# Kernel tuning notes

Hardware: AMD Instinct MI355X
Metric: run time of the kernel (lower is better)

## Reference

```python
import jax, jax.numpy as jnp
import numpy as np

N = 50000          # nodes
E = 800000         # edges (before self loops)
D_IN = 128         # input_dim
HID = 64           # hidden_dim (per head)
HEADS = 2
DM = HID * HEADS   # 128, post-concat dim
OUT = 32           # out_channels
G = 64             # graphs in batch
EPS = 1e-5
SLOPE = 0.2        # GATConv negative_slope default


def setup_inputs() -> dict:
    key = jax.random.key(0)
    ks = jax.random.split(key, 24)
    s = 0.1
    return {
        "x": jax.random.normal(ks[0], (N, D_IN), jnp.float32),
        "edge_index": jax.random.randint(ks[1], (2, E), 0, N, jnp.int32),
        "batch": jnp.sort(jax.random.randint(ks[2], (N,), 0, G, jnp.int32)),
        # GAT layer 1
        "W1": jax.random.normal(ks[3], (D_IN, DM), jnp.float32) * s,
        "att_src1": jax.random.normal(ks[4], (HEADS, HID), jnp.float32) * s,
        "att_dst1": jax.random.normal(ks[5], (HEADS, HID), jnp.float32) * s,
        "b1": jnp.zeros((DM,), jnp.float32),
        "ln1_g": jnp.ones((DM,), jnp.float32),
        "ln1_b": jnp.zeros((DM,), jnp.float32),
        # skip connection
        "Wskip": jax.random.normal(ks[6], (D_IN, DM), jnp.float32) * s,
        "bskip": jnp.zeros((DM,), jnp.float32),
        # GAT layer 2
        "W2": jax.random.normal(ks[7], (DM, DM), jnp.float32) * s,
        "att_src2": jax.random.normal(ks[8], (HEADS, HID), jnp.float32) * s,
        "att_dst2": jax.random.normal(ks[9], (HEADS, HID), jnp.float32) * s,
        "b2": jnp.zeros((DM,), jnp.float32),
        "ln2_g": jnp.ones((DM,), jnp.float32),
        "ln2_b": jnp.zeros((DM,), jnp.float32),
        # head
        "Wfc": jax.random.normal(ks[10], (DM, OUT), jnp.float32) * s,
        "bfc": jnp.zeros((OUT,), jnp.float32),
        "bn_g": jnp.ones((OUT,), jnp.float32),
        "bn_b": jnp.zeros((OUT,), jnp.float32),
    }


def _layer_norm(x, g, b):
    m = x.mean(-1, keepdims=True)
    v = ((x - m) ** 2).mean(-1, keepdims=True)
    return (x - m) * jax.lax.rsqrt(v + EPS) * g + b


def _gat(h_in, W, att_src, att_dst, bias, src, dst):
    # PyG GATConv (concat=True): h = x W reshaped to [N,H,C]
    h = (h_in @ W).reshape(N, HEADS, HID)
    a_src = (h * att_src).sum(-1)   # [N,H]
    a_dst = (h * att_dst).sum(-1)   # [N,H]
    e = jax.nn.leaky_relu(a_src[src] + a_dst[dst], SLOPE)  # [E',H]
    # segment softmax over edges sharing target node
    e = e - jax.ops.segment_max(e, dst, num_segments=N)[dst]
    ee = jnp.exp(e)
    denom = jax.ops.segment_sum(ee, dst, num_segments=N)[dst]
    alpha = ee / denom
    msg = h[src] * alpha[:, :, None]               # [E',H,C]
    out = jax.ops.segment_sum(msg, dst, num_segments=N)  # [N,H,C]
    return out.reshape(N, DM) + bias


def reference(x, edge_index, batch, W1, att_src1, att_dst1, b1, ln1_g, ln1_b,
              Wskip, bskip, W2, att_src2, att_dst2, b2, ln2_g, ln2_b,
              Wfc, bfc, bn_g, bn_b):
    # add self loops (PyG GATConv default)
    loop = jnp.arange(N, dtype=edge_index.dtype)
    src = jnp.concatenate([edge_index[0], loop])
    dst = jnp.concatenate([edge_index[1], loop])

    x1 = _gat(x, W1, att_src1, att_dst1, b1, src, dst)
    x1 = jax.nn.elu(_layer_norm(x1, ln1_g, ln1_b))
    x1 = x1 + (x @ Wskip + bskip)          # dropout = identity (eval)

    x2 = _gat(x1, W2, att_src2, att_dst2, b2, src, dst)
    x2 = _layer_norm(x2 + x1, ln2_g, ln2_b)
    emb = jax.nn.elu(x2)

    # global mean pool per graph
    sums = jax.ops.segment_sum(emb, batch, num_segments=G)
    cnt = jax.ops.segment_sum(jnp.ones((N,), emb.dtype), batch, num_segments=G)
    graph_emb = sums / jnp.maximum(cnt, 1.0)[:, None]

    logits = graph_emb @ Wfc + bfc
    # BatchNorm1d (training-mode batch stats, biased var)
    m = logits.mean(0)
    v = ((logits - m) ** 2).mean(0)
    return (logits - m) * jax.lax.rsqrt(v + EPS) * bn_g + bn_b
```

## Files before the change

### kernel.cpp

```cpp
#include <hip/hip_runtime.h>

#define DM    128
#define NHEAD 2
#define HIDC  64
#define OUTC  32
#define NG    64
#define EPS   1e-5f
#define DCAP  64

typedef __attribute__((ext_vector_type(8))) short bf16x8;
typedef __attribute__((ext_vector_type(4))) float f32x4;

__device__ __forceinline__ unsigned short f2bf(float f) {
    union { float f; unsigned int u; } v; v.f = f;
    unsigned int r = v.u + 0x7fffu + ((v.u >> 16) & 1u);
    return (unsigned short)(r >> 16);
}
__device__ __forceinline__ float bflo(unsigned int u) {
    union { unsigned int u; float f; } v; v.u = u << 16; return v.f;
}
__device__ __forceinline__ float bfhi(unsigned int u) {
    union { unsigned int u; float f; } v; v.u = u & 0xffff0000u; return v.f;
}

__global__ __launch_bounds__(256) void build_prep_kernel(
    const int* __restrict__ ei, int E, int eb,
    int* __restrict__ cursor, unsigned short* __restrict__ col,
    const float* __restrict__ W1, const float* __restrict__ Wskip,
    const float* __restrict__ W2,
    unsigned short* __restrict__ wf1, unsigned short* __restrict__ wfs,
    unsigned short* __restrict__ wf2,
    const float* __restrict__ x, unsigned short* __restrict__ xbf, int total)
{
    const int b = blockIdx.x;
    if (b < eb) {
        const int e = b * 256 + threadIdx.x;
        if (e < E) {
            const int d = ei[E + e];
            const int k = atomicAdd(&cursor[d], 1);
            if (k < DCAP) col[d * DCAP + k] = (unsigned short)ei[e];
        }
    } else if (b < eb + 24) {
        const int wb = b - eb;
        const float* W = wb < 8 ? W1 : (wb < 16 ? Wskip : W2);
        unsigned short* WF = wb < 8 ? wf1 : (wb < 16 ? wfs : wf2);
        const int idx = (wb & 7) * 256 + threadIdx.x;
        const int nt   = idx >> 8;
        const int ks   = (idx >> 6) & 3;
        const int lane = idx & 63;
        const int c    = nt * 16 + (lane & 15);
        const int k0   = ks * 32 + (lane >> 4) * 8;
        bf16x8 f;
#pragma unroll
        for (int j = 0; j < 8; ++j)
            f[j] = (short)f2bf(W[(k0 + j) * DM + c]);
        ((bf16x8*)WF)[idx] = f;
    } else {
        const int i = ((b - eb - 24) * 256 + threadIdx.x) * 4;
        if (i < total) {
            const float4 v = *(const float4*)&x[i];
            ushort4 o;
            o.x = f2bf(v.x); o.y = f2bf(v.y); o.z = f2bf(v.z); o.w = f2bf(v.w);
            *(ushort4*)&xbf[i] = o;
        }
    }
}

__device__ __forceinline__ void gemm_body(
    const unsigned short* __restrict__ Xbf, int N,
    const unsigned short* __restrict__ Wfrag,
    const float* __restrict__ bias,
    const float* __restrict__ att_src,
    const float* __restrict__ att_dst,
    float* __restrict__ C,
    unsigned short* __restrict__ Cbf,
    float* __restrict__ a_src,
    float* __restrict__ a_dst,
    int bid, int nblocks)
{
    const int lane = threadIdx.x & 63;
    const int wave = threadIdx.x >> 6;
    const int col  = lane & 15;
    const int kgrp = lane >> 4;

    bf16x8 bfrag[8][4];
    {
        const bf16x8* wf = (const bf16x8*)Wfrag;
#pragma unroll
        for (int nt = 0; nt < 8; ++nt)
#pragma unroll
            for (int ks = 0; ks < 4; ++ks)
                bfrag[nt][ks] = wf[(nt * 4 + ks) * 64 + lane];
    }

    float bcol[8];
#pragma unroll
    for (int nt = 0; nt < 8; ++nt)
        bcol[nt] = bias ? bias[nt * 16 + col] : 0.f;

    float as_c[8], ad_c[8];
    if (att_src) {
#pragma unroll
        for (int nt = 0; nt < 8; ++nt) {
            as_c[nt] = att_src[nt * 16 + col];
            ad_c[nt] = att_dst[nt * 16 + col];
        }
    }

    const int ntiles = (N + 15) >> 4;
    for (int tile = bid * 4 + wave; tile < ntiles; tile += nblocks * 4) {
        const int row0 = tile * 16;

        f32x4 acc[8];
#pragma unroll
        for (int nt = 0; nt < 8; ++nt) acc[nt] = (f32x4){0.f, 0.f, 0.f, 0.f};

        const int r = min(row0 + col, N - 1);
#pragma unroll
        for (int ks = 0; ks < 4; ++ks) {
            const int k0 = ks * 32 + kgrp * 8;
            const bf16x8 af = *(const bf16x8*)&Xbf[(size_t)r * DM + k0];
#pragma unroll
            for (int nt = 0; nt < 8; ++nt)
                acc[nt] = __builtin_amdgcn_mfma_f32_16x16x32_bf16(
                              af, bfrag[nt][ks], acc[nt], 0, 0, 0);
        }

        float dots[4][2], dotd[4][2];
        if (att_src) {
#pragma unroll
            for (int reg = 0; reg < 4; ++reg) {
                dots[reg][0] = dots[reg][1] = 0.f;
                dotd[reg][0] = dotd[reg][1] = 0.f;
            }
        }
#pragma unroll
        for (int reg = 0; reg < 4; ++reg) {
            const int row = row0 + kgrp * 4 + reg;
            const bool ok = row < N;
#pragma unroll
            for (int nt = 0; nt < 8; ++nt) {
                const float o = acc[nt][reg] + bcol[nt];
                if (ok) {
                    if (Cbf) Cbf[(size_t)row * DM + nt * 16 + col] = f2bf(o);
                    else     C  [(size_t)row * DM + nt * 16 + col] = o;
                }
                if (att_src) {
                    dots[reg][nt >> 2] += o * as_c[nt];
                    dotd[reg][nt >> 2] += o * ad_c[nt];
                }
            }
        }
        if (att_src) {
#pragma unroll
            for (int reg = 0; reg < 4; ++reg) {
#pragma unroll
                for (int h = 0; h < 2; ++h) {
                    float vs = dots[reg][h], vd = dotd[reg][h];
#pragma unroll
                    for (int off = 8; off; off >>= 1) {
                        vs += __shfl_xor(vs, off);
                        vd += __shfl_xor(vd, off);
                    }
                    const int row = row0 + kgrp * 4 + reg;
                    if (col == 0 && row < N) {
                        a_src[row * NHEAD + h] = vs;
                        a_dst[row * NHEAD + h] = vd;
                    }
                }
            }
        }
    }
}

__global__ __launch_bounds__(256) void gemm_pair_kernel(
    const unsigned short* __restrict__ Xbf, int N,
    const unsigned short* __restrict__ wf1,
    const unsigned short* __restrict__ wfs,
    const float* __restrict__ bskip,
    const float* __restrict__ as1, const float* __restrict__ ad1,
    unsigned short* __restrict__ Hbuf, float* __restrict__ Skip,
    float* __restrict__ a_src, float* __restrict__ a_dst)
{
    if (blockIdx.x < 256)
        gemm_body(Xbf, N, wf1, nullptr, as1, ad1, nullptr, Hbuf,
                  a_src, a_dst, blockIdx.x, 256);
    else
        gemm_body(Xbf, N, wfs, bskip, nullptr, nullptr, Skip, nullptr,
                  nullptr, nullptr, blockIdx.x - 256, 256);
}

__global__ __launch_bounds__(256) void mfma_gemm_kernel(
    const unsigned short* __restrict__ Xbf, int N,
    const unsigned short* __restrict__ Wfrag,
    const float* __restrict__ att_src,
    const float* __restrict__ att_dst,
    unsigned short* __restrict__ Cbf,
    float* __restrict__ a_src,
    float* __restrict__ a_dst)
{
    gemm_body(Xbf, N, Wfrag, nullptr, att_src, att_dst, nullptr, Cbf,
              a_src, a_dst, blockIdx.x, gridDim.x);
}

__global__ __launch_bounds__(128) void gat_agg_ln_kernel(
    const int* __restrict__ deg,
    const unsigned short* __restrict__ col,
    const unsigned short* __restrict__ H,
    const float* __restrict__ a_src,
    const float* __restrict__ a_dst,
    const float* __restrict__ bias,
    const unsigned short* __restrict__ res,
    const float* __restrict__ lng,
    const float* __restrict__ lnb,
    const float* __restrict__ skip,
    unsigned short* __restrict__ obf,
    int N)
{
    const int wid  = threadIdx.x >> 6;
    const int d    = blockIdx.x * 2 + wid;
    if (d >= N) return;
    const int lane = threadIdx.x & 63;
    const int half = lane >> 5;
    const int c2   = lane * 2;

    const float ad_h = a_dst[d * NHEAD + half];

    float e0 = a_src[d * NHEAD + half] + ad_h;
    e0 = e0 > 0.f ? e0 : 0.2f * e0;
    const float wself = __expf(e0);
    float den = wself;
    float2 acc;
    {
        const unsigned int hu = *(const unsigned int*)&H[(size_t)d * DM + c2];
        acc.x = wself * bflo(hu);
        acc.y = wself * bfhi(hu);
    }

    const int dg = min(deg[d], DCAP);
    const int p0 = d * DCAP;
    for (int base = 0; base < dg; base += 32) {
        const int m = min(32, dg - base);
        const int el = lane & 31;

        float we = 0.f;
        int s = 0;
        if (el < m) {
            s = (int)col[p0 + base + el];
            float a = a_src[s * NHEAD + half] + ad_h;
            a = a > 0.f ? a : 0.2f * a;
            we = __expf(a);
        }
        float ws = we;
#pragma unroll
        for (int off = 1; off < 32; off <<= 1) ws += __shfl_xor(ws, off);
        den += ws;

        const int hsel = lane & 32;
        int e = 0;
        for (; e + 4 <= m; e += 4) {
            const int s0 = __shfl(s, e),     s1 = __shfl(s, e + 1);
            const int s2 = __shfl(s, e + 2), s3 = __shfl(s, e + 3);
            const float w0 = __shfl(we, hsel | e),       w1 = __shfl(we, hsel | (e + 1));
            const float w2 = __shfl(we, hsel | (e + 2)), w3 = __shfl(we, hsel | (e + 3));
            const unsigned int u0 = *(const unsigned int*)&H[(size_t)s0 * DM + c2];
            const unsigned int u1 = *(const unsigned int*)&H[(size_t)s1 * DM + c2];
            const unsigned int u2 = *(const unsigned int*)&H[(size_t)s2 * DM + c2];
            const unsigned int u3 = *(const unsigned int*)&H[(size_t)s3 * DM + c2];
            acc.x += w0 * bflo(u0) + w1 * bflo(u1) + w2 * bflo(u2) + w3 * bflo(u3);
            acc.y += w0 * bfhi(u0) + w1 * bfhi(u1) + w2 * bfhi(u2) + w3 * bfhi(u3);
        }
        for (; e < m; ++e) {
            const int sE = __shfl(s, e);
            const float wE = __shfl(we, hsel | e);
            const unsigned int uE = *(const unsigned int*)&H[(size_t)sE * DM + c2];
            acc.x += wE * bflo(uE);
            acc.y += wE * bfhi(uE);
        }
    }

    const size_t ibase = (size_t)d * DM + c2;
    const float2 bv = *(const float2*)&bias[c2];
    float vx = acc.x / den + bv.x;
    float vy = acc.y / den + bv.y;
    if (res) {
        const unsigned int ru = *(const unsigned int*)&res[ibase];
        vx += bflo(ru); vy += bfhi(ru);
    }

    float sm = vx + vy;
#pragma unroll
    for (int off = 1; off < 64; off <<= 1) sm += __shfl_xor(sm, off);
    const float mean = sm * (1.f / DM);

    const float dx = vx - mean, dy = vy - mean;
    float s2 = dx * dx + dy * dy;
#pragma unroll
    for (int off = 1; off < 64; off <<= 1) s2 += __shfl_xor(s2, off);
    const float rstd = rsqrtf(s2 * (1.f / DM) + EPS);

    const float2 gv = *(const float2*)&lng[c2];
    const float2 bb = *(const float2*)&lnb[c2];
    float yx = dx * rstd * gv.x + bb.x;
    float yy = dy * rstd * gv.y + bb.y;
    yx = yx > 0.f ? yx : expm1f(yx);
    yy = yy > 0.f ? yy : expm1f(yy);
    if (skip) {
        const float2 sk = *(const float2*)&skip[ibase];
        yx += sk.x; yy += sk.y;
    }
    const unsigned int pk = (unsigned int)f2bf(yx) |
                            ((unsigned int)f2bf(yy) << 16);
    *(unsigned int*)&obf[ibase] = pk;
}

__global__ void pool_kernel(const unsigned short* __restrict__ emb,
                            const int* __restrict__ batch, int N,
                            float* __restrict__ sums,
                            float* __restrict__ cnt)
{
    const int t = threadIdx.x;
    const int chunk = (N + gridDim.x - 1) / gridDim.x;
    const int n0 = blockIdx.x * chunk;
    const int n1 = min(N, n0 + chunk);
    if (n0 >= n1) return;

    int cur = batch[n0];
    float acc = 0.f;
    int count = 0;
    for (int n = n0; n < n1; ++n) {
        int b = batch[n];
        if (b != cur) {
            atomicAdd(&sums[cur * DM + t], acc);
            if (t == 0) atomicAdd(&cnt[cur], (float)count);
            acc = 0.f; count = 0; cur = b;
        }
        unsigned short h = emb[(size_t)n * DM + t];
        union { unsigned int u; float f; } v; v.u = ((unsigned int)h) << 16;
        acc += v.f;
        ++count;
    }
    atomicAdd(&sums[cur * DM + t], acc);
    if (t == 0) atomicAdd(&cnt[cur], (float)count);
}

__global__ void head_kernel(const float* __restrict__ sums,
                            const float* __restrict__ cnt,
                            const float* __restrict__ Wfc,
                            const float* __restrict__ bfc,
                            const float* __restrict__ bn_g,
                            const float* __restrict__ bn_b,
                            float* __restrict__ out)
{
    __shared__ float ge[NG * DM];
    __shared__ float lg[NG * OUTC];
    __shared__ float mu[OUTC], inv[OUTC];
    const int t = threadIdx.x;

    for (int i = t; i < NG * DM; i += blockDim.x) {
        int g = i >> 7;
        ge[i] = sums[i] / fmaxf(cnt[g], 1.0f);
    }
    __syncthreads();

    for (int i = t; i < NG * OUTC; i += blockDim.x) {
        int g = i >> 5, o = i & (OUTC - 1);
        float acc = bfc[o];
#pragma unroll
        for (int k = 0; k < DM; ++k) acc += ge[g * DM + k] * Wfc[k * OUTC + o];
        lg[i] = acc;
    }
    __syncthreads();

    if (t < OUTC) {
        float s = 0.f;
        for (int g = 0; g < NG; ++g) s += lg[g * OUTC + t];
        float m = s * (1.f / NG);
        float v = 0.f;
        for (int g = 0; g < NG; ++g) { float d = lg[g * OUTC + t] - m; v += d * d; }
        v *= (1.f / NG);
        mu[t] = m;
        inv[t] = rsqrtf(v + EPS) * bn_g[t];
    }
    __syncthreads();

    for (int i = t; i < NG * OUTC; i += blockDim.x) {
        int o = i & (OUTC - 1);
        out[i] = (lg[i] - mu[o]) * inv[o] + bn_b[o];
    }
}

extern "C" void kernel_launch(void* const* d_in, const int* in_sizes, int n_in,
                              void* d_out, int out_size, void* d_ws, size_t ws_size,
                              hipStream_t stream)
{
    const float* x     = (const float*)d_in[0];
    const int*   ei    = (const int*)  d_in[1];
    const int*   batch = (const int*)  d_in[2];
    const float* W1    = (const float*)d_in[3];
    const float* as1   = (const float*)d_in[4];
    const float* ad1   = (const float*)d_in[5];
    const float* b1    = (const float*)d_in[6];
    const float* ln1g  = (const float*)d_in[7];
    const float* ln1b  = (const float*)d_in[8];
    const float* Wskip = (const float*)d_in[9];
    const float* bskip = (const float*)d_in[10];
    const float* W2    = (const float*)d_in[11];
    const float* as2   = (const float*)d_in[12];
    const float* ad2   = (const float*)d_in[13];
    const float* b2    = (const float*)d_in[14];
    const float* ln2g  = (const float*)d_in[15];
    const float* ln2b  = (const float*)d_in[16];
    const float* Wfc   = (const float*)d_in[17];
    const float* bfc   = (const float*)d_in[18];
    const float* bng   = (const float*)d_in[19];
    const float* bnb   = (const float*)d_in[20];

    const int N  = in_sizes[2];
    const int E  = in_sizes[1] / 2;

    size_t off = 0;
    auto alloc = [&](size_t bytes) -> char* {
        char* p = (char*)d_ws + off;
        off += (bytes + 255) & ~(size_t)255;
        return p;
    };
    unsigned short* Hbuf   = (unsigned short*)alloc((size_t)N * DM * 2);
    unsigned short* xbf    = (unsigned short*)alloc((size_t)N * DM * 2);
    unsigned short* Buf1bf = (unsigned short*)alloc((size_t)N * DM * 2);
    unsigned short* Buf2bf = (unsigned short*)alloc((size_t)N * DM * 2);
    float* Skip   = (float*)alloc((size_t)N * DM * 4);
    float* asrc   = (float*)alloc((size_t)N * NHEAD * 4);
    float* adst   = (float*)alloc((size_t)N * NHEAD * 4);
    int*   cursor = (int*)  alloc((size_t)N * 4);
    unsigned short* col = (unsigned short*)alloc((size_t)N * DCAP * 2);
    unsigned short* wf1 = (unsigned short*)alloc((size_t)2048 * 8 * 2);
    unsigned short* wfs = (unsigned short*)alloc((size_t)2048 * 8 * 2);
    unsigned short* wf2 = (unsigned short*)alloc((size_t)2048 * 8 * 2);
    float* sums   = (float*)alloc((size_t)(NG * DM + NG) * 4);
    float* cnt    = sums + NG * DM;

    const int eb = (E + 255) / 256;
    const int ab = (N + 1) / 2;
    const int xb = (N * DM / 4 + 255) / 256;

    hipMemsetAsync(cursor, 0, (size_t)N * 4, stream);
    build_prep_kernel<<<eb + 24 + xb, 256, 0, stream>>>(
        ei, E, eb, cursor, col, W1, Wskip, W2, wf1, wfs, wf2,
        x, xbf, N * DM);

    gemm_pair_kernel<<<512, 256, 0, stream>>>(xbf, N, wf1, wfs, bskip,
                                              as1, ad1, Hbuf, Skip, asrc, adst);
    gat_agg_ln_kernel<<<ab, 128, 0, stream>>>(cursor, col, Hbuf, asrc, adst,
                                              b1, nullptr, ln1g, ln1b, Skip,
                                              Buf1bf, N);

    mfma_gemm_kernel<<<256, 256, 0, stream>>>(Buf1bf, N, wf2, as2, ad2,
                                              Hbuf, asrc, adst);
    gat_agg_ln_kernel<<<ab, 128, 0, stream>>>(cursor, col, Hbuf, asrc, adst,
                                              b2, Buf1bf, ln2g, ln2b, nullptr,
                                              Buf2bf, N);

    hipMemsetAsync(sums, 0, (size_t)(NG * DM + NG) * 4, stream);
    pool_kernel<<<1024, DM, 0, stream>>>(Buf2bf, batch, N, sums, cnt);
    head_kernel<<<1, 1024, 0, stream>>>(sums, cnt, Wfc, bfc, bng, bnb, (float*)d_out);
}
```

Baseline: 226.7 us.

## Fold memsets into prep kernel, move edge scatter into GEMM launch, bf16 skip

The two hipMemsetAsync calls are replaced by zeroing blocks inside the prep kernel. The edge-to-CSR scatter moves out of the prep launch and into the first GEMM launch, so the atomics overlap with the MFMA work. The skip-connection output is now stored as bf16 instead of fp32, which halves its write and read traffic at some cost in precision. Fewer launches and less memory traffic are the intended gains; the scatter now shares compute units with the GEMM blocks.

```diff
diff --git a/kernel.cpp b/kernel.cpp
--- a/kernel.cpp
+++ b/kernel.cpp
@@ -23,28 +23,20 @@
     union { unsigned int u; float f; } v; v.u = u & 0xffff0000u; return v.f;
 }
 
-__global__ __launch_bounds__(256) void build_prep_kernel(
-    const int* __restrict__ ei, int E, int eb,
-    int* __restrict__ cursor, unsigned short* __restrict__ col,
+__global__ __launch_bounds__(256) void prep_kernel(
     const float* __restrict__ W1, const float* __restrict__ Wskip,
     const float* __restrict__ W2,
     unsigned short* __restrict__ wf1, unsigned short* __restrict__ wfs,
     unsigned short* __restrict__ wf2,
-    const float* __restrict__ x, unsigned short* __restrict__ xbf, int total)
+    const float* __restrict__ x, unsigned short* __restrict__ xbf, int total,
+    int xb, int* __restrict__ cursor, int N,
+    float* __restrict__ sums, int sums_n, int cz)
 {
     const int b = blockIdx.x;
-    if (b < eb) {
-        const int e = b * 256 + threadIdx.x;
-        if (e < E) {
-            const int d = ei[E + e];
-            const int k = atomicAdd(&cursor[d], 1);
-            if (k < DCAP) col[d * DCAP + k] = (unsigned short)ei[e];
-        }
-    } else if (b < eb + 24) {
-        const int wb = b - eb;
-        const float* W = wb < 8 ? W1 : (wb < 16 ? Wskip : W2);
-        unsigned short* WF = wb < 8 ? wf1 : (wb < 16 ? wfs : wf2);
-        const int idx = (wb & 7) * 256 + threadIdx.x;
+    if (b < 24) {
+        const float* W = b < 8 ? W1 : (b < 16 ? Wskip : W2);
+        unsigned short* WF = b < 8 ? wf1 : (b < 16 ? wfs : wf2);
+        const int idx = (b & 7) * 256 + threadIdx.x;
         const int nt   = idx >> 8;
         const int ks   = (idx >> 6) & 3;
         const int lane = idx & 63;
@@ -55,14 +47,24 @@
         for (int j = 0; j < 8; ++j)
             f[j] = (short)f2bf(W[(k0 + j) * DM + c]);
         ((bf16x8*)WF)[idx] = f;
-    } else {
-        const int i = ((b - eb - 24) * 256 + threadIdx.x) * 4;
+    } else if (b < 24 + xb) {
+        const int i = ((b - 24) * 256 + threadIdx.x) * 4;
         if (i < total) {
             const float4 v = *(const float4*)&x[i];
             ushort4 o;
             o.x = f2bf(v.x); o.y = f2bf(v.y); o.z = f2bf(v.z); o.w = f2bf(v.w);
             *(ushort4*)&xbf[i] = o;
         }
+    } else if (b < 24 + xb + cz) {
+        const int i0 = ((b - 24 - xb) * 256 + threadIdx.x) * 4;
+#pragma unroll
+        for (int k = 0; k < 4; ++k)
+            if (i0 + k < N) cursor[i0 + k] = 0;
+    } else {
+        const int i0 = ((b - 24 - xb - cz) * 256 + threadIdx.x) * 4;
+#pragma unroll
+        for (int k = 0; k < 4; ++k)
+            if (i0 + k < sums_n) sums[i0 + k] = 0.f;
     }
 }
 
@@ -72,7 +74,6 @@
     const float* __restrict__ bias,
     const float* __restrict__ att_src,
     const float* __restrict__ att_dst,
-    float* __restrict__ C,
     unsigned short* __restrict__ Cbf,
     float* __restrict__ a_src,
     float* __restrict__ a_dst,
@@ -141,10 +142,7 @@
 #pragma unroll
             for (int nt = 0; nt < 8; ++nt) {
                 const float o = acc[nt][reg] + bcol[nt];
-                if (ok) {
-                    if (Cbf) Cbf[(size_t)row * DM + nt * 16 + col] = f2bf(o);
-                    else     C  [(size_t)row * DM + nt * 16 + col] = o;
-                }
+                if (ok) Cbf[(size_t)row * DM + nt * 16 + col] = f2bf(o);
                 if (att_src) {
                     dots[reg][nt >> 2] += o * as_c[nt];
                     dotd[reg][nt >> 2] += o * ad_c[nt];
@@ -173,21 +171,31 @@
     }
 }
 
-__global__ __launch_bounds__(256) void gemm_pair_kernel(
+__global__ __launch_bounds__(256) void gemm_scatter_kernel(
     const unsigned short* __restrict__ Xbf, int N,
     const unsigned short* __restrict__ wf1,
     const unsigned short* __restrict__ wfs,
     const float* __restrict__ bskip,
     const float* __restrict__ as1, const float* __restrict__ ad1,
-    unsigned short* __restrict__ Hbuf, float* __restrict__ Skip,
-    float* __restrict__ a_src, float* __restrict__ a_dst)
-{
-    if (blockIdx.x < 256)
-        gemm_body(Xbf, N, wf1, nullptr, as1, ad1, nullptr, Hbuf,
-                  a_src, a_dst, blockIdx.x, 256);
-    else
-        gemm_body(Xbf, N, wfs, bskip, nullptr, nullptr, Skip, nullptr,
-                  nullptr, nullptr, blockIdx.x - 256, 256);
+    unsigned short* __restrict__ Hbuf, unsigned short* __restrict__ Skipbf,
+    float* __restrict__ a_src, float* __restrict__ a_dst,
+    const int* __restrict__ ei, int E,
+    int* __restrict__ cursor, unsigned short* __restrict__ col)
+{
+    const int b = blockIdx.x;
+    if (b < 256) {
+        gemm_body(Xbf, N, wf1, nullptr, as1, ad1, Hbuf, a_src, a_dst, b, 256);
+    } else if (b < 512) {
+        gemm_body(Xbf, N, wfs, bskip, nullptr, nullptr, Skipbf,
+                  nullptr, nullptr, b - 256, 256);
+    } else {
+        const int e = (b - 512) * 256 + threadIdx.x;
+        if (e < E) {
+            const int d = ei[E + e];
+            const int k = atomicAdd(&cursor[d], 1);
+            if (k < DCAP) col[d * DCAP + k] = (unsigned short)ei[e];
+        }
+    }
 }
 
 __global__ __launch_bounds__(256) void mfma_gemm_kernel(
@@ -199,7 +207,7 @@
     float* __restrict__ a_src,
     float* __restrict__ a_dst)
 {
-    gemm_body(Xbf, N, Wfrag, nullptr, att_src, att_dst, nullptr, Cbf,
+    gemm_body(Xbf, N, Wfrag, nullptr, att_src, att_dst, Cbf,
               a_src, a_dst, blockIdx.x, gridDim.x);
 }
 
@@ -213,7 +221,7 @@
     const unsigned short* __restrict__ res,
     const float* __restrict__ lng,
     const float* __restrict__ lnb,
-    const float* __restrict__ skip,
+    const unsigned short* __restrict__ skip,
     unsigned short* __restrict__ obf,
     int N)
 {
@@ -306,8 +314,8 @@
     yx = yx > 0.f ? yx : expm1f(yx);
     yy = yy > 0.f ? yy : expm1f(yy);
     if (skip) {
-        const float2 sk = *(const float2*)&skip[ibase];
-        yx += sk.x; yy += sk.y;
+        const unsigned int su = *(const unsigned int*)&skip[ibase];
+        yx += bflo(su); yy += bfhi(su);
     }
     const unsigned int pk = (unsigned int)f2bf(yx) |
                             ((unsigned int)f2bf(yy) << 16);
@@ -429,7 +437,7 @@
     unsigned short* xbf    = (unsigned short*)alloc((size_t)N * DM * 2);
     unsigned short* Buf1bf = (unsigned short*)alloc((size_t)N * DM * 2);
     unsigned short* Buf2bf = (unsigned short*)alloc((size_t)N * DM * 2);
-    float* Skip   = (float*)alloc((size_t)N * DM * 4);
+    unsigned short* Skipbf = (unsigned short*)alloc((size_t)N * DM * 2);
     float* asrc   = (float*)alloc((size_t)N * NHEAD * 4);
     float* adst   = (float*)alloc((size_t)N * NHEAD * 4);
     int*   cursor = (int*)  alloc((size_t)N * 4);
@@ -443,16 +451,20 @@
     const int eb = (E + 255) / 256;
     const int ab = (N + 1) / 2;
     const int xb = (N * DM / 4 + 255) / 256;
-
-    hipMemsetAsync(cursor, 0, (size_t)N * 4, stream);
-    build_prep_kernel<<<eb + 24 + xb, 256, 0, stream>>>(
-        ei, E, eb, cursor, col, W1, Wskip, W2, wf1, wfs, wf2,
-        x, xbf, N * DM);
-
-    gemm_pair_kernel<<<512, 256, 0, stream>>>(xbf, N, wf1, wfs, bskip,
-                                              as1, ad1, Hbuf, Skip, asrc, adst);
+    const int cz = (N + 1023) / 1024;
+    const int sums_n = NG * DM + NG;
+    const int sz = (sums_n + 1023) / 1024;
+
+    prep_kernel<<<24 + xb + cz + sz, 256, 0, stream>>>(
+        W1, Wskip, W2, wf1, wfs, wf2, x, xbf, N * DM, xb,
+        cursor, N, sums, sums_n, cz);
+
+    gemm_scatter_kernel<<<512 + eb, 256, 0, stream>>>(
+        xbf, N, wf1, wfs, bskip, as1, ad1, Hbuf, Skipbf, asrc, adst,
+        ei, E, cursor, col);
+
     gat_agg_ln_kernel<<<ab, 128, 0, stream>>>(cursor, col, Hbuf, asrc, adst,
-                                              b1, nullptr, ln1g, ln1b, Skip,
+                                              b1, nullptr, ln1g, ln1b, Skipbf,
                                               Buf1bf, N);
 
     mfma_gemm_kernel<<<256, 256, 0, stream>>>(Buf1bf, N, wf2, as2, ad2,
@@ -461,7 +473,6 @@
                                               b2, Buf1bf, ln2g, ln2b, nullptr,
                                               Buf2bf, N);
 
-    hipMemsetAsync(sums, 0, (size_t)(NG * DM + NG) * 4, stream);
     pool_kernel<<<1024, DM, 0, stream>>>(Buf2bf, batch, N, sums, cnt);
     head_kernel<<<1, 1024, 0, stream>>>(sums, cnt, Wfc, bfc, bng, bnb, (float*)d_out);
 }
```

Result: faster. 205.5 us, median of 2 (-9.3%).
